# Performance work log

Measured on AMD Instinct MI355X. Metric: run time of the kernel, lower is better.

Reference implementation:

```python
import jax, jax.numpy as jnp
import numpy as np

N, E = 50000, 800000
IN_FEATS, HIDDEN, HEADS, NUM_CLASSES, EDGE_FEAT = 64, 64, 4, 4, 2
D_HEAD = HIDDEN // HEADS


def _lin(key, fan_in, fan_out):
    k1, k2 = jax.random.split(key)
    s = 1.0 / np.sqrt(fan_in)
    W = jax.random.uniform(k1, (fan_in, fan_out), jnp.float32, -s, s)
    b = jax.random.uniform(k2, (fan_out,), jnp.float32, -s, s)
    return W, b


def setup_inputs() -> dict:
    key = jax.random.key(0)
    ks = jax.random.split(key, 10)
    x = jax.random.normal(ks[0], (N, IN_FEATS), jnp.float32)
    edge_index = jax.random.randint(ks[1], (2, E), 0, N, jnp.int32)
    edge_attr = jax.random.normal(ks[2], (E, EDGE_FEAT), jnp.float32)
    Wn, bn = _lin(ks[3], IN_FEATS, HIDDEN)
    We, be = _lin(ks[4], EDGE_FEAT, HIDDEN)
    Wq, bq = _lin(ks[5], HIDDEN, HIDDEN)
    Wk, bk = _lin(ks[6], HIDDEN, HIDDEN)
    Wv, bv = _lin(ks[7], HIDDEN, HIDDEN)
    Ws, bs = _lin(ks[8], HIDDEN, HIDDEN)   # lin_skip (root weight)
    Wf, bf = _lin(ks[9], HIDDEN, NUM_CLASSES)
    return {"x": x, "edge_index": edge_index, "edge_attr": edge_attr,
            "Wn": Wn, "bn": bn, "We": We, "be": be,
            "Wq": Wq, "bq": bq, "Wk": Wk, "bk": bk, "Wv": Wv, "bv": bv,
            "Ws": Ws, "bs": bs, "Wf": Wf, "bf": bf}


def _segment_softmax(logits, seg, num_segments):
    # logits: [E, H], seg: [E] destination node ids
    m = jax.ops.segment_max(logits, seg, num_segments=num_segments)  # [N, H]
    m = jnp.where(jnp.isfinite(m), m, 0.0)
    e = jnp.exp(logits - m[seg])
    s = jax.ops.segment_sum(e, seg, num_segments=num_segments)
    return e / (s[seg] + 1e-16)


def reference(x, edge_index, edge_attr, Wn, bn, We, be, Wq, bq, Wk, bk, Wv, bv, Ws, bs, Wf, bf):
    src, dst = edge_index[0], edge_index[1]
    h = x @ Wn + bn                                   # [N, HIDDEN]
    ea = (edge_attr @ We + be).reshape(E, HEADS, D_HEAD)
    q = (h @ Wq + bq).reshape(N, HEADS, D_HEAD)
    k = (h @ Wk + bk).reshape(N, HEADS, D_HEAD)
    v = (h @ Wv + bv).reshape(N, HEADS, D_HEAD)
    # per-edge attention logits (PyG flow source_to_target: query at dst, key at src)
    logits = jnp.einsum('ehd,ehd->eh', q[dst], k[src]) / np.sqrt(D_HEAD)
    alpha = _segment_softmax(logits, dst, N)          # [E, H]
    # edge_attr added to values (lin_edge is None since edge_dim not set)
    msg = (v[src] + ea) * alpha[:, :, None]           # [E, H, D]
    out = jax.ops.segment_sum(msg, dst, num_segments=N).reshape(N, HIDDEN)
    out = out + h @ Ws + bs                           # root/skip connection
    # dropout is identity in eval mode
    edge_out = out[src] + out[dst]                    # [E, HIDDEN]
    return edge_out @ Wf + bf                         # [E, NUM_CLASSES]
```

## Files before the change

### kernel.cpp

```cpp
#include <hip/hip_runtime.h>
#include <hip/hip_bf16.h>
#include <hip/hip_fp16.h>

#define N_NODES 50000
#define N_EDGES 800000
#define NB_T64 ((N_NODES + 63) / 64)
#define WT_BLOCKS 16
#define CAP 64

#define BIN_SHIFT 8
#define NBINS ((N_NODES + 255) / 256)
#define CAP_BIN 5120
#define EPB 2048
#define NB_BIN ((N_EDGES + EPB - 1) / EPB)

typedef unsigned short u16;
typedef unsigned int   u32;
typedef __attribute__((ext_vector_type(8))) short short8;
typedef __attribute__((ext_vector_type(8))) unsigned short ushort8;
typedef __attribute__((ext_vector_type(4))) float f32x4;

__device__ __forceinline__ float bf2f(u16 u) {
    union { u32 i; float f; } z; z.i = ((u32)u) << 16; return z.f;
}
__device__ __forceinline__ u16 f2bf(float f) {
    union { float f; u32 i; } z; z.f = f;
    u32 x = z.i;
    u32 r = (x + 0x7fffu + ((x >> 16) & 1u)) >> 16;
    return (u16)r;
}
__device__ __forceinline__ float h2f(u16 u) {
    __half h; *(u16*)&h = u; return __half2float(h);
}
__device__ __forceinline__ u16 f2h(float f) {
    __half h = __float2half_rn(f);
    return *(u16*)&h;
}
__device__ __forceinline__ float ldf(const void* p, size_t i, bool isbf) {
    return isbf ? bf2f(((const u16*)p)[i]) : ((const float*)p)[i];
}
__device__ __forceinline__ u16 ldbf(const void* p, size_t i, bool isbf) {
    return isbf ? ((const u16*)p)[i] : f2bf(((const float*)p)[i]);
}

#define WSB_COUNT 772

__global__ __launch_bounds__(256) void k_init(
    const void* __restrict__ Wn, const void* __restrict__ bn,
    const void* __restrict__ Wq, const void* __restrict__ bq,
    const void* __restrict__ Wk, const void* __restrict__ bk,
    const void* __restrict__ Wv, const void* __restrict__ bv,
    const void* __restrict__ Ws, const void* __restrict__ bs,
    const void* __restrict__ We, const void* __restrict__ be,
    const void* __restrict__ Wf, const void* __restrict__ bfv,
    const int* __restrict__ ei, const void* __restrict__ ea,
    u16* __restrict__ wsT, float* __restrict__ wsB,
    uint2* __restrict__ bins, u32* __restrict__ gcur,
    const int isbf)
{
    const int t = threadIdx.x, bid = blockIdx.x;
    if (bid >= WT_BLOCKS) {
        __shared__ u32 h[NBINS];
        __shared__ u32 off[NBINS];
        const int blk = bid - WT_BLOCKS;
        const int e0 = blk * EPB + t * 8;
        const bool vec = (e0 + 8 <= N_EDGES);
        int dv[8];
        if (vec) {
            const int4 a = *(const int4*)(ei + N_EDGES + e0);
            const int4 b = *(const int4*)(ei + N_EDGES + e0 + 4);
            dv[0] = a.x; dv[1] = a.y; dv[2] = a.z; dv[3] = a.w;
            dv[4] = b.x; dv[5] = b.y; dv[6] = b.z; dv[7] = b.w;
        } else {
            #pragma unroll
            for (int j = 0; j < 8; ++j)
                dv[j] = (e0 + j < N_EDGES) ? ei[N_EDGES + e0 + j] : -1;
        }
        if (t < NBINS) { h[t] = 0; off[t] = 0; }
        __syncthreads();
        #pragma unroll
        for (int j = 0; j < 8; ++j)
            if (dv[j] >= 0) atomicAdd(&h[dv[j] >> BIN_SHIFT], 1u);
        __syncthreads();
        if (t < NBINS && h[t] != 0) h[t] = atomicAdd(&gcur[t], h[t]);
        __syncthreads();
        int sv[8];
        if (vec) {
            const int4 a = *(const int4*)(ei + e0);
            const int4 b = *(const int4*)(ei + e0 + 4);
            sv[0] = a.x; sv[1] = a.y; sv[2] = a.z; sv[3] = a.w;
            sv[4] = b.x; sv[5] = b.y; sv[6] = b.z; sv[7] = b.w;
        } else {
            #pragma unroll
            for (int j = 0; j < 8; ++j)
                sv[j] = (e0 + j < N_EDGES) ? ei[e0 + j] : 0;
        }
        #pragma unroll
        for (int j = 0; j < 8; ++j) {
            if (dv[j] < 0) continue;
            const int e = e0 + j;
            float ea0, ea1;
            if (isbf) {
                const u32 w2 = ((const u32*)ea)[e];
                ea0 = bf2f((u16)(w2 & 0xffffu));
                ea1 = bf2f((u16)(w2 >> 16));
            } else {
                const float2 f2 = ((const float2*)ea)[e];
                ea0 = f2.x; ea1 = f2.y;
            }
            const __half2 hh = __floats2half2_rn(ea0, ea1);
            const int b = dv[j] >> BIN_SHIFT;
            const u32 rank = atomicAdd(&off[b], 1u);
            const u32 slot = h[b] + rank;
            if (slot < CAP_BIN) {
                uint2 r;
                r.x = (u32)sv[j] | ((u32)dv[j] << 16);
                r.y = *(const u32*)&hh;
                bins[(size_t)b * CAP_BIN + slot] = r;
            }
        }
        return;
    }

    const int i = bid * 256 + t;
    {
        const int kk = i >> 6, n = i & 63;
        const int o = n * 64 + kk;
        wsT[0 * 4096 + o] = ldbf(Wn, i, isbf);
        wsT[1 * 4096 + o] = ldbf(Wq, i, isbf);
        wsT[2 * 4096 + o] = ldbf(Wk, i, isbf);
        wsT[3 * 4096 + o] = ldbf(Wv, i, isbf);
        wsT[4 * 4096 + o] = ldbf(Ws, i, isbf);
    }
    if (bid == 0) {
        if (t < 64) {
            wsB[t]       = ldf(bn, t, isbf);
            wsB[64 + t]  = ldf(bq, t, isbf);
            wsB[128 + t] = ldf(bk, t, isbf);
            wsB[192 + t] = ldf(bv, t, isbf);
            wsB[256 + t] = ldf(bs, t, isbf);
            wsB[320 + t] = ldf(We, t, isbf);
            wsB[384 + t] = ldf(We, 64 + t, isbf);
            wsB[448 + t] = ldf(be, t, isbf);
        }
        wsB[512 + t] = ldf(Wf, t, isbf);
        if (t < 4) wsB[768 + t] = ldf(bfv, t, isbf);
    }
}

__global__ __launch_bounds__(512, 4) void k_bn(
    const void* __restrict__ x,
    const u16* __restrict__ wsT, const float* __restrict__ wsB,
    const uint2* __restrict__ bins, const u32* __restrict__ gcur,
    int* __restrict__ deg, uint2* __restrict__ rec,
    u16* __restrict__ qbf, u16* __restrict__ kvbf,
    u16* __restrict__ obf, const int isbf)
{
    __shared__ u16 xs[2 * 32 * 72];
    const int t = threadIdx.x, bid = blockIdx.x;

    if (bid < NBINS) {
        __shared__ u32 cnt[1 << BIN_SHIFT];
        const int lo = bid << BIN_SHIFT;
        const int rsz = (N_NODES - lo < (1 << BIN_SHIFT)) ? (N_NODES - lo)
                                                          : (1 << BIN_SHIFT);
        for (int i = t; i < (1 << BIN_SHIFT); i += 512) cnt[i] = 0;
        __syncthreads();
        int n = (int)gcur[bid];
        if (n > CAP_BIN) n = CAP_BIN;
        const uint2* bp = bins + (size_t)bid * CAP_BIN;
        for (int i = t; i < n; i += 512) {
            const uint2 r = bp[i];
            const u32 d = r.x >> 16;
            const u32 rank = atomicAdd(&cnt[d - (u32)lo], 1u) & (u32)(CAP - 1);
            uint2 o;
            o.x = r.x & 0xffffu;
            o.y = r.y;
            rec[((size_t)d << 6) + rank] = o;
        }
        __syncthreads();
        for (int i = t; i < rsz; i += 512) deg[lo + i] = (int)cnt[i];
        return;
    }

    const int tt = t & 255, half = t >> 8;
    const int w = tt >> 6, lane = tt & 63;
    const int l15 = lane & 15, quad = lane >> 4;
    const int base = (bid - NBINS) * 64 + half * 32;
    u16* xh = xs + half * (32 * 72);

    {
        const int m = tt >> 3, kc = tt & 7;
        const int node = base + m;
        short8 vd = {0, 0, 0, 0, 0, 0, 0, 0};
        if (node < N_NODES) {
            if (isbf) {
                vd = *(const short8*)((const u16*)x + (size_t)node * 64 + kc * 8);
            } else {
                const float4 f0 = *(const float4*)((const float*)x + (size_t)node * 64 + kc * 8);
                const float4 f1 = *(const float4*)((const float*)x + (size_t)node * 64 + kc * 8 + 4);
                vd[0] = f2bf(f0.x); vd[1] = f2bf(f0.y);
                vd[2] = f2bf(f0.z); vd[3] = f2bf(f0.w);
                vd[4] = f2bf(f1.x); vd[5] = f2bf(f1.y);
                vd[6] = f2bf(f1.z); vd[7] = f2bf(f1.w);
            }
        }
        *(short8*)(xh + m * 72 + kc * 8) = vd;
    }
    short8 b1[2][4];
    if (w < 2) {
        #pragma unroll
        for (int ks = 0; ks < 2; ++ks)
            #pragma unroll
            for (int nt = 0; nt < 4; ++nt)
                b1[ks][nt] = *(const short8*)(wsT + (nt * 16 + l15) * 64 + ks * 32 + quad * 8);
    }
    __syncthreads();

    if (w < 2) {
        f32x4 acc1[4];
        #pragma unroll
        for (int nt = 0; nt < 4; ++nt) acc1[nt] = (f32x4){0.f, 0.f, 0.f, 0.f};
        #pragma unroll
        for (int ks = 0; ks < 2; ++ks) {
            const short8 a = *(const short8*)(xh + (w * 16 + l15) * 72 + ks * 32 + quad * 8);
            #pragma unroll
            for (int nt = 0; nt < 4; ++nt)
                acc1[nt] = __builtin_amdgcn_mfma_f32_16x16x32_bf16(a, b1[ks][nt], acc1[nt], 0, 0, 0);
        }
        #pragma unroll
        for (int nt = 0; nt < 4; ++nt)
            #pragma unroll
            for (int r = 0; r < 4; ++r) {
                const int m = w * 16 + quad * 4 + r;
                const int col = nt * 16 + l15;
                xh[m * 72 + col] = f2bf(acc1[nt][r] + wsB[col]);
            }
    }
    short8 b2[2][4];
    {
        const u16* wt = wsT + (w + 1) * 4096;
        #pragma unroll
        for (int ks = 0; ks < 2; ++ks)
            #pragma unroll
            for (int nt = 0; nt < 4; ++nt)
                b2[ks][nt] = *(const short8*)(wt + (nt * 16 + l15) * 64 + ks * 32 + quad * 8);
    }
    __syncthreads();

    {
        f32x4 acc2[2][4];
        #pragma unroll
        for (int mt = 0; mt < 2; ++mt)
            #pragma unroll
            for (int nt = 0; nt < 4; ++nt) acc2[mt][nt] = (f32x4){0.f, 0.f, 0.f, 0.f};
        #pragma unroll
        for (int ks = 0; ks < 2; ++ks) {
            short8 a[2];
            #pragma unroll
            for (int mt = 0; mt < 2; ++mt)
                a[mt] = *(const short8*)(xh + (mt * 16 + l15) * 72 + ks * 32 + quad * 8);
            #pragma unroll
            for (int nt = 0; nt < 4; ++nt)
                #pragma unroll
                for (int mt = 0; mt < 2; ++mt)
                    acc2[mt][nt] = __builtin_amdgcn_mfma_f32_16x16x32_bf16(a[mt], b2[ks][nt], acc2[mt][nt], 0, 0, 0);
        }
        const float* bias = wsB + 64 + w * 64;
        #pragma unroll
        for (int mt = 0; mt < 2; ++mt)
            #pragma unroll
            for (int nt = 0; nt < 4; ++nt)
                #pragma unroll
                for (int r = 0; r < 4; ++r) {
                    const int node = base + mt * 16 + quad * 4 + r;
                    if (node >= N_NODES) continue;
                    const int col = nt * 16 + l15;
                    const float v = acc2[mt][nt][r] + bias[col];
                    if (w == 1) {
                        kvbf[(size_t)node * 128 + ((col >> 2) << 3) + (col & 3)] = f2h(v);
                    } else if (w == 2) {
                        kvbf[(size_t)node * 128 + ((col >> 2) << 3) + 4 + (col & 3)] = f2h(v);
                    } else if (w == 0) {
                        qbf[(size_t)node * 64 + col] = f2h(v);
                    } else {
                        obf[(size_t)node * 64 + col] = f2bf(v);
                    }
                }
    }
}

__global__ __launch_bounds__(256) void k_agg(
    const int* __restrict__ deg,
    const uint2* __restrict__ rec,
    const u16* __restrict__ qbf, const u16* __restrict__ kvbf,
    const u16* __restrict__ obf,
    const float* __restrict__ wsB,
    float4* __restrict__ y)
{
    const int wid = (blockIdx.x * 256 + threadIdx.x) >> 6;
    const int lane = threadIdx.x & 63;
    if (wid >= N_NODES) return;
    const int d = wid;
    const int lg = lane & 15;
    const int g  = lane >> 4;

    const ushort4 q4u = *(const ushort4*)(qbf + (size_t)d * 64 + lg * 4);
    const ushort4 o4  = *(const ushort4*)(obf + (size_t)d * 64 + lg * 4);
    const float q0 = h2f(q4u.x), q1 = h2f(q4u.y);
    const float q2 = h2f(q4u.z), q3 = h2f(q4u.w);

    const int beg = d << 6;
    int dg = deg[d];
    dg = (dg > CAP) ? CAP : dg;

    float den = 0.f, sa0 = 0.f, sa1 = 0.f;
    float av0 = 0.f, av1 = 0.f, av2 = 0.f, av3 = 0.f;

    const u16* kvp = kvbf + lg * 8;
    for (int j = 0; j < dg; j += 16) {
        uint2 rr[4];
        #pragma unroll
        for (int qq = 0; qq < 4; ++qq)
            rr[qq] = rec[beg + j + 4 * qq + g];
        ushort8 kv[4];
        #pragma unroll
        for (int qq = 0; qq < 4; ++qq) {
            const bool valid = (j + 4 * qq + g) < dg;
            const u32 rx = valid ? rr[qq].x : 0u;
            kv[qq] = *(const ushort8*)(kvp + (size_t)rx * 128);
        }
        #pragma unroll
        for (int qq = 0; qq < 4; ++qq) {
            const bool valid = (j + 4 * qq + g) < dg;
            float prod =      h2f(kv[qq][0]) * q0;
            prod = fmaf(h2f(kv[qq][1]), q1, prod);
            prod = fmaf(h2f(kv[qq][2]), q2, prod);
            prod = fmaf(h2f(kv[qq][3]), q3, prod);
            prod += __shfl_xor(prod, 1, 64);
            prod += __shfl_xor(prod, 2, 64);
            float ex = __expf(prod * 0.25f);
            ex = valid ? ex : 0.f;
            const u32 ry = valid ? rr[qq].y : 0u;
            const u16 el = (u16)(ry & 0xffffu), eh = (u16)(ry >> 16);
            den += ex;
            sa0 = fmaf(ex, h2f(el), sa0);
            sa1 = fmaf(ex, h2f(eh), sa1);
            av0 = fmaf(ex, h2f(kv[qq][4]), av0);
            av1 = fmaf(ex, h2f(kv[qq][5]), av1);
            av2 = fmaf(ex, h2f(kv[qq][6]), av2);
            av3 = fmaf(ex, h2f(kv[qq][7]), av3);
        }
    }
    #pragma unroll
    for (int o = 16; o < 64; o <<= 1) {
        den += __shfl_xor(den, o, 64);
        sa0 += __shfl_xor(sa0, o, 64);
        sa1 += __shfl_xor(sa1, o, 64);
        av0 += __shfl_xor(av0, o, 64);
        av1 += __shfl_xor(av1, o, 64);
        av2 += __shfl_xor(av2, o, 64);
        av3 += __shfl_xor(av3, o, 64);
    }

    const float4 we04 = *(const float4*)(wsB + 320 + lg * 4);
    const float4 we14 = *(const float4*)(wsB + 384 + lg * 4);
    const float4 bef4 = *(const float4*)(wsB + 448 + lg * 4);
    const float rden = 1.0f / (den + 1e-16f);
    const float res0 = bf2f(o4.x) + (av0 + we04.x * sa0 + we14.x * sa1 + bef4.x * den) * rden;
    const float res1 = bf2f(o4.y) + (av1 + we04.y * sa0 + we14.y * sa1 + bef4.y * den) * rden;
    const float res2 = bf2f(o4.z) + (av2 + we04.z * sa0 + we14.z * sa1 + bef4.z * den) * rden;
    const float res3 = bf2f(o4.w) + (av3 + we04.w * sa0 + we14.w * sa1 + bef4.w * den) * rden;

    const float4 wf0 = *(const float4*)(wsB + 512 + (lg * 4 + 0) * 4);
    const float4 wf1 = *(const float4*)(wsB + 512 + (lg * 4 + 1) * 4);
    const float4 wf2 = *(const float4*)(wsB + 512 + (lg * 4 + 2) * 4);
    const float4 wf3 = *(const float4*)(wsB + 512 + (lg * 4 + 3) * 4);
    float y0 = res0 * wf0.x + res1 * wf1.x + res2 * wf2.x + res3 * wf3.x;
    float y1 = res0 * wf0.y + res1 * wf1.y + res2 * wf2.y + res3 * wf3.y;
    float y2 = res0 * wf0.z + res1 * wf1.z + res2 * wf2.z + res3 * wf3.z;
    float y3 = res0 * wf0.w + res1 * wf1.w + res2 * wf2.w + res3 * wf3.w;
    #pragma unroll
    for (int o = 1; o < 16; o <<= 1) {
        y0 += __shfl_xor(y0, o, 64);
        y1 += __shfl_xor(y1, o, 64);
        y2 += __shfl_xor(y2, o, 64);
        y3 += __shfl_xor(y3, o, 64);
    }
    if (lane == 0) {
        float4 yv;
        yv.x = y0 + 0.5f * wsB[768];
        yv.y = y1 + 0.5f * wsB[769];
        yv.z = y2 + 0.5f * wsB[770];
        yv.w = y3 + 0.5f * wsB[771];
        y[d] = yv;
    }
}

__global__ __launch_bounds__(256) void k_edgeout(
    const int* __restrict__ ei,
    const float4* __restrict__ y,
    void* __restrict__ out, const int isbf)
{
    const int idx = blockIdx.x * 256 + threadIdx.x;
    const int e0 = idx * 2;
    if (e0 >= N_EDGES) return;
    const int2 ss = *(const int2*)(ei + e0);
    const int2 dd = *(const int2*)(ei + N_EDGES + e0);
    const float4 ya = y[ss.x], yb = y[dd.x];
    const float4 yc = y[ss.y], yd = y[dd.y];
    const float a0 = ya.x + yb.x, a1 = ya.y + yb.y;
    const float a2 = ya.z + yb.z, a3 = ya.w + yb.w;
    const float c0 = yc.x + yd.x, c1 = yc.y + yd.y;
    const float c2 = yc.z + yd.z, c3 = yc.w + yd.w;
    if (isbf) {
        uint4 r;
        r.x = (u32)f2bf(a0) | ((u32)f2bf(a1) << 16);
        r.y = (u32)f2bf(a2) | ((u32)f2bf(a3) << 16);
        r.z = (u32)f2bf(c0) | ((u32)f2bf(c1) << 16);
        r.w = (u32)f2bf(c2) | ((u32)f2bf(c3) << 16);
        *(uint4*)((u16*)out + (size_t)e0 * 4) = r;
    } else {
        float4 r0; r0.x = a0; r0.y = a1; r0.z = a2; r0.w = a3;
        float4 r1; r1.x = c0; r1.y = c1; r1.z = c2; r1.w = c3;
        *(float4*)((float*)out + (size_t)e0 * 4) = r0;
        *(float4*)((float*)out + (size_t)e0 * 4 + 4) = r1;
    }
}

extern "C" void kernel_launch(void* const* d_in, const int* in_sizes, int n_in,
                              void* d_out, int out_size, void* d_ws, size_t ws_size,
                              hipStream_t stream)
{
    (void)n_in; (void)out_size; (void)ws_size;
    const void* x   = d_in[0];
    const int*  ei  = (const int*)d_in[1];
    const void* ea  = d_in[2];
    const void* Wn  = d_in[3];  const void* bn  = d_in[4];
    const void* We  = d_in[5];  const void* be  = d_in[6];
    const void* Wq  = d_in[7];  const void* bq  = d_in[8];
    const void* Wk  = d_in[9];  const void* bk  = d_in[10];
    const void* Wv  = d_in[11]; const void* bv  = d_in[12];
    const void* Ws_ = d_in[13]; const void* bs  = d_in[14];
    const void* Wf  = d_in[15]; const void* bfv = d_in[16];

    const int isbf = (in_sizes[0] == N_NODES * 64 * 2) ? 1 : 0;

    char*   wsp   = (char*)d_ws;
    uint2*  rec   = (uint2*)wsp;
    float4* y     = (float4*)(rec + (size_t)N_NODES * CAP);
    u16*    qbf   = (u16*)(y + N_NODES);
    u16*    kvbf  = qbf + (size_t)N_NODES * 64;
    u16*    obf   = kvbf + (size_t)N_NODES * 128;
    u16*    wsT   = obf + (size_t)N_NODES * 64;
    float*  wsB   = (float*)(wsT + 5 * 4096);
    int*    deg   = (int*)(wsB + WSB_COUNT);
    uint2*  bins  = (uint2*)(deg + N_NODES);
    u32*    gcur  = (u32*)(bins + (size_t)NBINS * CAP_BIN);

    hipMemsetAsync(gcur, 0, NBINS * sizeof(u32), stream);
    k_init<<<WT_BLOCKS + NB_BIN, 256, 0, stream>>>(
        Wn, bn, Wq, bq, Wk, bk, Wv, bv, Ws_, bs, We, be, Wf, bfv, ei, ea,
        wsT, wsB, bins, gcur, isbf);
    k_bn<<<NBINS + NB_T64, 512, 0, stream>>>(x, wsT, wsB, bins, gcur,
                                             deg, rec, qbf, kvbf, obf, isbf);
    k_agg<<<(N_NODES * 64 + 255) / 256, 256, 0, stream>>>(deg, rec, qbf, kvbf,
                                                          obf, wsB, y);
    k_edgeout<<<(N_EDGES / 2 + 255) / 256, 256, 0, stream>>>(ei, y, d_out, isbf);
}
```

Before: 200.6 us.

## Map four nodes per wave in aggregation with sequential edge loop and prefetch

```diff
diff --git a/kernel.cpp b/kernel.cpp
--- a/kernel.cpp
+++ b/kernel.cpp
@@ -298,12 +298,12 @@
     const float* __restrict__ wsB,
     float4* __restrict__ y)
 {
-    const int wid = (blockIdx.x * 256 + threadIdx.x) >> 6;
     const int lane = threadIdx.x & 63;
-    if (wid >= N_NODES) return;
-    const int d = wid;
-    const int lg = lane & 15;
-    const int g  = lane >> 4;
+    const int wave = threadIdx.x >> 6;
+    const int sub = lane >> 4;
+    const int lg  = lane & 15;
+    const int d = blockIdx.x * 16 + wave * 4 + sub;
+    if (d >= N_NODES) return;
 
     const ushort4 q4u = *(const ushort4*)(qbf + (size_t)d * 64 + lg * 4);
     const ushort4 o4  = *(const ushort4*)(obf + (size_t)d * 64 + lg * 4);
@@ -317,50 +317,30 @@
     float den = 0.f, sa0 = 0.f, sa1 = 0.f;
     float av0 = 0.f, av1 = 0.f, av2 = 0.f, av3 = 0.f;
 
-    const u16* kvp = kvbf + lg * 8;
-    for (int j = 0; j < dg; j += 16) {
-        uint2 rr[4];
-        #pragma unroll
-        for (int qq = 0; qq < 4; ++qq)
-            rr[qq] = rec[beg + j + 4 * qq + g];
-        ushort8 kv[4];
-        #pragma unroll
-        for (int qq = 0; qq < 4; ++qq) {
-            const bool valid = (j + 4 * qq + g) < dg;
-            const u32 rx = valid ? rr[qq].x : 0u;
-            kv[qq] = *(const ushort8*)(kvp + (size_t)rx * 128);
-        }
-        #pragma unroll
-        for (int qq = 0; qq < 4; ++qq) {
-            const bool valid = (j + 4 * qq + g) < dg;
-            float prod =      h2f(kv[qq][0]) * q0;
-            prod = fmaf(h2f(kv[qq][1]), q1, prod);
-            prod = fmaf(h2f(kv[qq][2]), q2, prod);
-            prod = fmaf(h2f(kv[qq][3]), q3, prod);
+    if (dg > 0) {
+        const u16* kvp = kvbf + lg * 8;
+        uint2 r = rec[beg];
+        for (int j = 0; j < dg; ++j) {
+            const int nj = (j + 1 < dg) ? (j + 1) : j;
+            const uint2 rn = rec[beg + nj];
+            const ushort8 kv = *(const ushort8*)(kvp + (size_t)r.x * 128);
+            float prod =      h2f(kv[0]) * q0;
+            prod = fmaf(h2f(kv[1]), q1, prod);
+            prod = fmaf(h2f(kv[2]), q2, prod);
+            prod = fmaf(h2f(kv[3]), q3, prod);
             prod += __shfl_xor(prod, 1, 64);
             prod += __shfl_xor(prod, 2, 64);
-            float ex = __expf(prod * 0.25f);
-            ex = valid ? ex : 0.f;
-            const u32 ry = valid ? rr[qq].y : 0u;
-            const u16 el = (u16)(ry & 0xffffu), eh = (u16)(ry >> 16);
+            const float ex = __expf(prod * 0.25f);
+            const u16 el = (u16)(r.y & 0xffffu), eh = (u16)(r.y >> 16);
             den += ex;
             sa0 = fmaf(ex, h2f(el), sa0);
             sa1 = fmaf(ex, h2f(eh), sa1);
-            av0 = fmaf(ex, h2f(kv[qq][4]), av0);
-            av1 = fmaf(ex, h2f(kv[qq][5]), av1);
-            av2 = fmaf(ex, h2f(kv[qq][6]), av2);
-            av3 = fmaf(ex, h2f(kv[qq][7]), av3);
-        }
-    }
-    #pragma unroll
-    for (int o = 16; o < 64; o <<= 1) {
-        den += __shfl_xor(den, o, 64);
-        sa0 += __shfl_xor(sa0, o, 64);
-        sa1 += __shfl_xor(sa1, o, 64);
-        av0 += __shfl_xor(av0, o, 64);
-        av1 += __shfl_xor(av1, o, 64);
-        av2 += __shfl_xor(av2, o, 64);
-        av3 += __shfl_xor(av3, o, 64);
+            av0 = fmaf(ex, h2f(kv[4]), av0);
+            av1 = fmaf(ex, h2f(kv[5]), av1);
+            av2 = fmaf(ex, h2f(kv[6]), av2);
+            av3 = fmaf(ex, h2f(kv[7]), av3);
+            r = rn;
+        }
     }
 
     const float4 we04 = *(const float4*)(wsB + 320 + lg * 4);
@@ -387,7 +367,7 @@
         y2 += __shfl_xor(y2, o, 64);
         y3 += __shfl_xor(y3, o, 64);
     }
-    if (lane == 0) {
+    if (lg == 0) {
         float4 yv;
         yv.x = y0 + 0.5f * wsB[768];
         yv.y = y1 + 0.5f * wsB[769];
@@ -464,7 +444,7 @@
         wsT, wsB, bins, gcur, isbf);
     k_bn<<<NBINS + NB_T64, 512, 0, stream>>>(x, wsT, wsB, bins, gcur,
                                              deg, rec, qbf, kvbf, obf, isbf);
-    k_agg<<<(N_NODES * 64 + 255) / 256, 256, 0, stream>>>(deg, rec, qbf, kvbf,
-                                                          obf, wsB, y);
+    k_agg<<<(N_NODES + 15) / 16, 256, 0, stream>>>(deg, rec, qbf, kvbf,
+                                                   obf, wsB, y);
     k_edgeout<<<(N_EDGES / 2 + 255) / 256, 256, 0, stream>>>(ei, y, d_out, isbf);
 }
```

Result: no change. 199.0 us (-0.8%).
